# Kernel optimization log

Measured on AMD Instinct MI355X. Metric: run time of the kernel, lower is better.

## Reference

```python
import jax, jax.numpy as jnp
import numpy as np

CASCADES = 3
D, H, W = 64, 256, 256
HID = 8  # BasicBlock hidden channels


def fdiff(x, axis):
    """Forward difference D x along `axis` (last entry 0) == sparse dx/dy/dz matmul."""
    axis = axis % x.ndim
    pad = [(0, 0)] * x.ndim
    pad[axis] = (0, 1)
    return jnp.pad(jnp.diff(x, axis=axis), pad)


def fdiff_t(y, axis):
    """Exact transpose D^T y of fdiff: (D^T y)_0=-y_0, (D^T y)_j=y_{j-1}-y_j, (D^T y)_{n-1}=y_{n-2}."""
    axis = axis % y.ndim
    n = y.shape[axis]
    yl = jax.lax.slice_in_dim(y, 0, n - 1, axis=axis)  # y[0..n-2]
    pf = [(0, 0)] * y.ndim; pf[axis] = (1, 0)
    pb = [(0, 0)] * y.ndim; pb[axis] = (0, 1)
    return jnp.pad(yl, pf) - jnp.pad(yl, pb)


def conv3d(x, w, b):
    out = jax.lax.conv_general_dilated(
        x, w, window_strides=(1, 1, 1), padding='SAME',
        dimension_numbers=('NCDHW', 'OIDHW', 'NCDHW'))
    return out + b[None, :, None, None, None]


def basic_block(x, w1, b1, w2, b2):
    h = jax.nn.relu(conv3d(x, w1, b1))
    return conv3d(h, w2, b2), jnp.mean(jnp.abs(h))


def ite(t, sino):
    """BeijingGeometry stand-in: one SIRT-style step A^T(sino - A t)/D, A = sum over depth."""
    proj = jnp.sum(t, axis=2)               # [B,1,H,W]
    res = sino - proj
    return jnp.broadcast_to(res[:, :, None], t.shape) / t.shape[2]


def setup_inputs() -> dict:
    key = jax.random.key(0)
    ks = jax.random.split(key, 8)
    image = jax.random.normal(ks[0], (1, 1, D, H, W), dtype=jnp.float32)
    sino = jax.random.normal(ks[1], (1, 1, H, W), dtype=jnp.float32)
    # 4 BasicBlocks stacked on leading axis
    W1 = jax.random.normal(ks[2], (4, HID, 1, 3, 3, 3), dtype=jnp.float32) * 0.1
    B1 = jnp.zeros((4, HID), dtype=jnp.float32)
    W2 = jax.random.normal(ks[3], (4, 1, HID, 3, 3, 3), dtype=jnp.float32) * 0.1
    B2 = jnp.zeros((4, 1), dtype=jnp.float32)
    ntx = jnp.full((CASCADES,), -0.01, dtype=jnp.float32)
    nty = jnp.full((CASCADES,), -0.01, dtype=jnp.float32)
    ntz = jnp.full((CASCADES,), -0.01, dtype=jnp.float32)
    nt = jnp.full((CASCADES,), -0.1, dtype=jnp.float32)
    return {"image": image, "sino": sino, "W1": W1, "B1": B1, "W2": W2, "B2": B2,
            "ntx": ntx, "nty": nty, "ntz": ntz, "nt": nt}


def reference(image, sino, W1, B1, W2, B2, ntx, nty, ntz, nt):
    t = image
    p = q = s = jnp.float32(0.0)
    outs = [image]
    for c in range(CASCADES):
        z = t + ite(t, sino)
        pnew, _ = basic_block(fdiff(z, -1), W1[0], B1[0], W2[0], B2[0])  # d/dx (W axis)
        qnew, _ = basic_block(fdiff(z, -2), W1[1], B1[1], W2[1], B2[1])  # d/dy (H axis)
        snew, _ = basic_block(fdiff(z, -3), W1[2], B1[2], W2[2], B2[2])  # d/dz (D axis)
        znew, _ = basic_block(z, W1[3], B1[3], W2[3], B2[3])
        p = p + ntx[c] * (p - pnew)
        q = q + nty[c] * (q - qnew)
        s = s + ntz[c] * (s - snew)
        z_ = t + nt[c] * (t - znew)
        t = fdiff_t(p, -1) + fdiff_t(q, -2) + fdiff_t(s, -3) + z_
        outs.append(t)
    return jnp.stack(outs, axis=0)  # [cascades+1, B, 1, D, H, W]
```

## Files before the change

### kernel.cpp

```cpp
#include <hip/hip_runtime.h>

#define DD 64
#define HH 256
#define WW 256
#define HW (HH * WW)
#define NVOX (DD * HW)

#define TS 32
#define DR 36
#define HPH 40
#define CHB 16
#define NPF 6

typedef __fp16 half2v __attribute__((ext_vector_type(2)));

#if __has_builtin(__builtin_amdgcn_fdot2)
#define FDOT2(a, b, c) __builtin_amdgcn_fdot2((a), (b), (c), false)
#else
#define FDOT2(a, b, c) \
  fmaf((float)(a).x, (float)(b).x, fmaf((float)(a).y, (float)(b).y, (c)))
#endif

__global__ __launch_bounds__(256) void k_corr(const float* __restrict__ t,
                                              const float* __restrict__ sino,
                                              float* __restrict__ corr) {
  int idx = blockIdx.x * 256 + threadIdx.x;
  float s = 0.f;
#pragma unroll 8
  for (int d = 0; d < DD; ++d) s += t[d * HW + idx];
  corr[idx] = (sino[idx] - s) * (1.0f / DD);
}

__global__ __launch_bounds__(256, 4) void k_blocks(
    const float* __restrict__ t, const float* __restrict__ corr,
    float* __restrict__ p, float* __restrict__ q, float* __restrict__ s_,
    float* __restrict__ zb,
    const float* __restrict__ W1g, const float* __restrict__ B1g,
    const float* __restrict__ W2g, const float* __restrict__ B2g,
    const float* __restrict__ ntx, const float* __restrict__ nty,
    const float* __restrict__ ntz, const float* __restrict__ nt, int c) {
  __shared__ __align__(16) float dbuf[3][DR][DR];
  __shared__ __align__(16) __fp16 hbuf[8][34][HPH];
  __shared__ __align__(8) half2v wpkl[72];

  const int b = blockIdx.z & 3;
  const int D0 = (blockIdx.z >> 2) * CHB;
  const int Dend = (D0 + CHB < DD) ? (D0 + CHB) : DD;
  const int ty0 = blockIdx.y * TS;
  const int tx0 = blockIdx.x * TS;
  const int tid = threadIdx.x;
  const bool edgeT = (ty0 == 0) || (ty0 == HH - TS) || (tx0 == 0) || (tx0 == WW - TS);

  const float* w1 = W1g + b * 216;
  const float* w2 = W2g + b * 216;
  float b1[8];
#pragma unroll
  for (int ch = 0; ch < 8; ++ch) b1[ch] = B1g[b * 8 + ch];
  const float b2 = B2g[b];
  const float coef = (b == 0) ? ntx[c] : (b == 1) ? nty[c] : (b == 2) ? ntz[c] : nt[c];
  const float* prevBuf = (b == 0) ? p : (b == 1) ? q : (b == 2) ? s_ : t;
  float* outBuf = (b == 0) ? p : (b == 1) ? q : (b == 2) ? s_ : zb;
  const bool zeroPrev = (c == 0) && (b < 3);
  const int strideA = (b == 0) ? 1 : (b == 1) ? WW : HW;

  auto dslot = [](int f) { return (f + 6) % 3; };

  if (tid < 72) {
    int ch = tid / 9, pr = tid - ch * 9;
    const float* w = w2 + ch * 27 + pr * 3;
    half2v hv;
    hv.x = (__fp16)w[0];
    hv.y = (__fp16)w[1];
    wpkl[tid] = hv;
  }

  int cbt[NPF];
  float dC[NPF];
  unsigned mbits = 0;
#pragma unroll
  for (int k = 0; k < NPF; ++k) {
    int i = tid + k * 256;
    int iy = i / DR, ix = i - iy * DR;
    int gy = ty0 - 2 + iy, gx = tx0 - 2 + ix;
    bool inb = (i < DR * DR) && ((unsigned)gy < HH) && ((unsigned)gx < WW);
    int cb = gy * WW + gx;
    cbt[k] = cb;
    bool m;
    float d = 0.f;
    if (b == 0) {
      m = inb && (gx + 1 < WW);
      if (m) d = corr[cb + 1] - corr[cb];
    } else if (b == 1) {
      m = inb && (gy + 1 < HH);
      if (m) d = corr[cb + WW] - corr[cb];
    } else if (b == 2) {
      m = inb;
    } else {
      m = inb;
      if (m) d = corr[cb];
    }
    dC[k] = d;
    if (m) mbits |= (1u << k);
  }

  float pA0[NPF], pA1[NPF];

  auto issue_loads = [&](int f) {
    const bool fok = (f >= 0) && (f < DD) && (b != 2 || (f + 1 < DD));
    const int fb = f * HW;
#pragma unroll
    for (int k = 0; k < NPF; ++k) {
      pA0[k] = 0.f; pA1[k] = 0.f;
      if (fok && ((mbits >> k) & 1u)) {
        const float* base = t + fb + cbt[k];
        pA0[k] = base[0];
        if (b != 3) pA1[k] = base[strideA];
      }
    }
  };
  auto write_deriv = [&](int f) {
    float* dst = &dbuf[dslot(f)][0][0];
#pragma unroll
    for (int k = 0; k < NPF; ++k) {
      if (k < 5 || tid < (DR * DR - 5 * 256)) {
        float v = (b == 3) ? (pA0[k] + dC[k]) : ((pA1[k] - pA0[k]) + dC[k]);
        dst[tid + k * 256] = v;
      }
    }
  };

  auto conv1_patch = [&](const float* d0, const float* d1, const float* d2,
                         int jy, int jx, int ch0, int ch1) {
    float win[3][4][4];
#pragma unroll
    for (int r = 0; r < 4; ++r) {
      int off = (jy + r) * DR + jx;
      const float2* r0 = (const float2*)(d0 + off);
      const float2* r1 = (const float2*)(d1 + off);
      const float2* r2 = (const float2*)(d2 + off);
      float2 a, bb;
      a = r0[0]; bb = r0[1];
      win[0][r][0] = a.x; win[0][r][1] = a.y; win[0][r][2] = bb.x; win[0][r][3] = bb.y;
      a = r1[0]; bb = r1[1];
      win[1][r][0] = a.x; win[1][r][1] = a.y; win[1][r][2] = bb.x; win[1][r][3] = bb.y;
      a = r2[0]; bb = r2[1];
      win[2][r][0] = a.x; win[2][r][1] = a.y; win[2][r][2] = bb.x; win[2][r][3] = bb.y;
    }
    bool in00 = true, in01 = true, in10 = true, in11 = true;
    if (edgeT) {
      int gy0 = ty0 - 1 + jy, gx0 = tx0 - 1 + jx;
      in00 = ((unsigned)gy0 < HH) && ((unsigned)gx0 < WW);
      in01 = ((unsigned)gy0 < HH) && ((unsigned)(gx0 + 1) < WW);
      in10 = ((unsigned)(gy0 + 1) < HH) && ((unsigned)gx0 < WW);
      in11 = ((unsigned)(gy0 + 1) < HH) && ((unsigned)(gx0 + 1) < WW);
    }
#pragma unroll 2
    for (int ch = ch0; ch < ch1; ++ch) {
      float bia = b1[ch];
      float a00 = bia, a01 = bia, a10 = bia, a11 = bia;
      const float* wch = w1 + ch * 27;
#pragma unroll
      for (int kz = 0; kz < 3; ++kz)
#pragma unroll
        for (int ky = 0; ky < 3; ++ky)
#pragma unroll
          for (int kx = 0; kx < 3; ++kx) {
            float wv = wch[kz * 9 + ky * 3 + kx];
            a00 = fmaf(wv, win[kz][ky][kx], a00);
            a01 = fmaf(wv, win[kz][ky][kx + 1], a01);
            a10 = fmaf(wv, win[kz][ky + 1][kx], a10);
            a11 = fmaf(wv, win[kz][ky + 1][kx + 1], a11);
          }
      float r00 = fmaxf(a00, 0.f), r01 = fmaxf(a01, 0.f);
      float r10 = fmaxf(a10, 0.f), r11 = fmaxf(a11, 0.f);
      if (edgeT) {
        r00 = in00 ? r00 : 0.f;
        r01 = in01 ? r01 : 0.f;
        r10 = in10 ? r10 : 0.f;
        r11 = in11 ? r11 : 0.f;
      }
      half2v h0, h1;
      h0.x = (__fp16)r00; h0.y = (__fp16)r01;
      h1.x = (__fp16)r10; h1.y = (__fp16)r11;
      *(half2v*)&hbuf[ch][jy][jx] = h0;
      *(half2v*)&hbuf[ch][jy + 1][jx] = h1;
    }
  };

  auto comp_hidden = [&](int e) {
    const float* d0 = &dbuf[dslot(e - 1)][0][0];
    const float* d1 = &dbuf[dslot(e)][0][0];
    const float* d2 = &dbuf[dslot(e + 1)][0][0];
    {
      int prr = tid / 17, pcc = tid - prr * 17;
      conv1_patch(d0, d1, d2, prr * 2, pcc * 2, 0, 8);
    }
    if (tid < 132) {
      int m = tid >> 2, chp = (tid & 3) << 1;
      int pi = 256 + m;
      int prr = pi / 17, pcc = pi - prr * 17;
      conv1_patch(d0, d1, d2, prr * 2, pcc * 2, chp, chp + 2);
    }
  };

  const int txi = tid & 15, tyi = tid >> 4;
  const int px0 = txi * 2, py0 = tyi * 2;

  float aM[2][2], aC[2][2], aP[2][2];
#pragma unroll
  for (int i = 0; i < 2; ++i)
#pragma unroll
    for (int j = 0; j < 2; ++j) { aM[i][j] = b2; aC[i][j] = b2; aP[i][j] = b2; }

  issue_loads(D0 - 2); write_deriv(D0 - 2);
  issue_loads(D0 - 1); write_deriv(D0 - 1);
  issue_loads(D0);     write_deriv(D0);
  __syncthreads();

  for (int e = D0 - 1; e <= Dend; ++e) {
    const bool live = (e >= 0 && e < DD);
    issue_loads(e + 2);
    float2 pr0, pr1;
    pr0.x = pr0.y = pr1.x = pr1.y = 0.f;
    const int d = e - 1;
    const bool doStore = (e >= D0 + 1);
    if (doStore && !zeroPrev) {
      size_t v0 = (size_t)d * HW + (size_t)(ty0 + py0) * WW + tx0 + px0;
      pr0 = *(const float2*)&prevBuf[v0];
      pr1 = *(const float2*)&prevBuf[v0 + WW];
    }
    if (live) comp_hidden(e);
    __syncthreads();
    if (live) {
#pragma unroll 1
      for (int ch = 0; ch < 8; ++ch) {
        const float* wch = w2 + ch * 27;
        const half2v* wrow = &wpkl[ch * 9];
        half2v H0[4], HP[4];
        float c0[4], c1[4];
#pragma unroll
        for (int r = 0; r < 4; ++r) {
          const __fp16* hp = &hbuf[ch][py0 + r][px0];
          half2v h0 = *(const half2v*)hp;
          half2v h1 = *(const half2v*)(hp + 2);
          unsigned u0, u1;
          __builtin_memcpy(&u0, &h0, 4);
          __builtin_memcpy(&u1, &h1, 4);
          unsigned pm = (u1 << 16) | (u0 >> 16);
          half2v hpv;
          __builtin_memcpy(&hpv, &pm, 4);
          H0[r] = h0; HP[r] = hpv;
          c0[r] = (float)h1.x;
          c1[r] = (float)h1.y;
        }
#pragma unroll
        for (int ky = 0; ky < 3; ++ky)
#pragma unroll
          for (int i = 0; i < 2; ++i) {
            const int r = i + ky;
            const half2v hA = H0[r], hB = HP[r];
            const float s0 = c0[r], s1 = c1[r];
            {
              half2v wv = wrow[ky];
              float ws = wch[ky * 3 + 2];
              aP[i][0] = FDOT2(hA, wv, aP[i][0]);
              aP[i][0] = fmaf(ws, s0, aP[i][0]);
              aP[i][1] = FDOT2(hB, wv, aP[i][1]);
              aP[i][1] = fmaf(ws, s1, aP[i][1]);
            }
            {
              half2v wv = wrow[3 + ky];
              float ws = wch[9 + ky * 3 + 2];
              aC[i][0] = FDOT2(hA, wv, aC[i][0]);
              aC[i][0] = fmaf(ws, s0, aC[i][0]);
              aC[i][1] = FDOT2(hB, wv, aC[i][1]);
              aC[i][1] = fmaf(ws, s1, aC[i][1]);
            }
            {
              half2v wv = wrow[6 + ky];
              float ws = wch[18 + ky * 3 + 2];
              aM[i][0] = FDOT2(hA, wv, aM[i][0]);
              aM[i][0] = fmaf(ws, s0, aM[i][0]);
              aM[i][1] = FDOT2(hB, wv, aM[i][1]);
              aM[i][1] = fmaf(ws, s1, aM[i][1]);
            }
          }
      }
    }
    write_deriv(e + 2);
    if (doStore) {
      size_t v0 = (size_t)d * HW + (size_t)(ty0 + py0) * WW + tx0 + px0;
      float2 o0, o1;
      o0.x = pr0.x + coef * (pr0.x - aM[0][0]);
      o0.y = pr0.y + coef * (pr0.y - aM[0][1]);
      o1.x = pr1.x + coef * (pr1.x - aM[1][0]);
      o1.y = pr1.y + coef * (pr1.y - aM[1][1]);
      *(float2*)&outBuf[v0] = o0;
      *(float2*)&outBuf[v0 + WW] = o1;
    }
#pragma unroll
    for (int i = 0; i < 2; ++i)
#pragma unroll
      for (int j = 0; j < 2; ++j) {
        aM[i][j] = aC[i][j]; aC[i][j] = aP[i][j]; aP[i][j] = b2;
      }
    __syncthreads();
  }
}

__global__ __launch_bounds__(256) void k_combine(
    const float* __restrict__ p, const float* __restrict__ q,
    const float* __restrict__ s_, const float* __restrict__ zb,
    float* __restrict__ tn) {
  int idx = blockIdx.x * 256 + threadIdx.x;
  int x = idx & (WW - 1);
  int y = (idx >> 8) & (HH - 1);
  int d = idx >> 16;
  float v = zb[idx];
  v += (x > 0 ? p[idx - 1] : 0.f) - (x < WW - 1 ? p[idx] : 0.f);
  v += (y > 0 ? q[idx - WW] : 0.f) - (y < HH - 1 ? q[idx] : 0.f);
  v += (d > 0 ? s_[idx - HW] : 0.f) - (d < DD - 1 ? s_[idx] : 0.f);
  tn[idx] = v;
}

extern "C" void kernel_launch(void* const* d_in, const int* in_sizes, int n_in,
                              void* d_out, int out_size, void* d_ws, size_t ws_size,
                              hipStream_t stream) {
  const float* image = (const float*)d_in[0];
  const float* sino  = (const float*)d_in[1];
  const float* W1    = (const float*)d_in[2];
  const float* B1    = (const float*)d_in[3];
  const float* W2    = (const float*)d_in[4];
  const float* B2    = (const float*)d_in[5];
  const float* ntx   = (const float*)d_in[6];
  const float* nty   = (const float*)d_in[7];
  const float* ntz   = (const float*)d_in[8];
  const float* nt    = (const float*)d_in[9];
  float* out = (float*)d_out;

  float* corr = (float*)d_ws;
  float* p  = corr + HW;
  float* q  = p + NVOX;
  float* s_ = q + NVOX;
  float* zb = s_ + NVOX;

  hipMemcpyAsync(out, image, (size_t)NVOX * sizeof(float),
                 hipMemcpyDeviceToDevice, stream);

  for (int c = 0; c < 3; ++c) {
    const float* t = out + (size_t)c * NVOX;
    float* tn = out + (size_t)(c + 1) * NVOX;
    k_corr<<<HW / 256, 256, 0, stream>>>(t, sino, corr);
    k_blocks<<<dim3(WW / TS, HH / TS, 16), 256, 0, stream>>>(
        t, corr, p, q, s_, zb, W1, B1, W2, B2, ntx, nty, ntz, nt, c);
    k_combine<<<NVOX / 256, 256, 0, stream>>>(p, q, s_, zb, tn);
  }
}
```

Baseline: 972.0 us.

## Use 320-thread blocks so each thread computes one full conv1 patch

Raises the fused conv block size from 256 to 320 threads so that 289 threads each compute one 2x2 hidden patch for all 8 channels. This removes the uneven second pass in which 132 threads split the leftover patches across channel pairs. Only the first 256 threads do the second convolution and the stores, and the derivative staging loads are respread over 5 per-thread slots. It also switches the fp16 packing to the cvt_pkrtz intrinsic, which rounds toward zero instead of to nearest. The trade-off is 64 threads idle during conv2 and more register pressure from the new occupancy target in launch_bounds.

```diff
diff --git a/kernel.cpp b/kernel.cpp
--- a/kernel.cpp
+++ b/kernel.cpp
@@ -10,7 +10,8 @@
 #define DR 36
 #define HPH 40
 #define CHB 16
-#define NPF 6
+#define NT 320
+#define NPF 5
 
 typedef __fp16 half2v __attribute__((ext_vector_type(2)));
 
@@ -31,7 +32,7 @@
   corr[idx] = (sino[idx] - s) * (1.0f / DD);
 }
 
-__global__ __launch_bounds__(256, 4) void k_blocks(
+__global__ __launch_bounds__(NT, 5) void k_blocks(
     const float* __restrict__ t, const float* __restrict__ corr,
     float* __restrict__ p, float* __restrict__ q, float* __restrict__ s_,
     float* __restrict__ zb,
@@ -49,6 +50,7 @@
   const int ty0 = blockIdx.y * TS;
   const int tx0 = blockIdx.x * TS;
   const int tid = threadIdx.x;
+  const bool owner = (tid < 256);
   const bool edgeT = (ty0 == 0) || (ty0 == HH - TS) || (tx0 == 0) || (tx0 == WW - TS);
 
   const float* w1 = W1g + b * 216;
@@ -79,7 +81,7 @@
   unsigned mbits = 0;
 #pragma unroll
   for (int k = 0; k < NPF; ++k) {
-    int i = tid + k * 256;
+    int i = tid + k * NT;
     int iy = i / DR, ix = i - iy * DR;
     int gy = ty0 - 2 + iy, gx = tx0 - 2 + ix;
     bool inb = (i < DR * DR) && ((unsigned)gy < HH) && ((unsigned)gx < WW);
@@ -122,15 +124,15 @@
     float* dst = &dbuf[dslot(f)][0][0];
 #pragma unroll
     for (int k = 0; k < NPF; ++k) {
-      if (k < 5 || tid < (DR * DR - 5 * 256)) {
+      if (k < NPF - 1 || tid < (DR * DR - (NPF - 1) * NT)) {
         float v = (b == 3) ? (pA0[k] + dC[k]) : ((pA1[k] - pA0[k]) + dC[k]);
-        dst[tid + k * 256] = v;
+        dst[tid + k * NT] = v;
       }
     }
   };
 
   auto conv1_patch = [&](const float* d0, const float* d1, const float* d2,
-                         int jy, int jx, int ch0, int ch1) {
+                         int jy, int jx) {
     float win[3][4][4];
 #pragma unroll
     for (int r = 0; r < 4; ++r) {
@@ -155,7 +157,7 @@
       in11 = ((unsigned)(gy0 + 1) < HH) && ((unsigned)(gx0 + 1) < WW);
     }
 #pragma unroll 2
-    for (int ch = ch0; ch < ch1; ++ch) {
+    for (int ch = 0; ch < 8; ++ch) {
       float bia = b1[ch];
       float a00 = bia, a01 = bia, a10 = bia, a11 = bia;
       const float* wch = w1 + ch * 27;
@@ -179,31 +181,22 @@
         r10 = in10 ? r10 : 0.f;
         r11 = in11 ? r11 : 0.f;
       }
-      half2v h0, h1;
-      h0.x = (__fp16)r00; h0.y = (__fp16)r01;
-      h1.x = (__fp16)r10; h1.y = (__fp16)r11;
-      *(half2v*)&hbuf[ch][jy][jx] = h0;
-      *(half2v*)&hbuf[ch][jy + 1][jx] = h1;
+      *(half2v*)&hbuf[ch][jy][jx]     = __builtin_amdgcn_cvt_pkrtz(r00, r01);
+      *(half2v*)&hbuf[ch][jy + 1][jx] = __builtin_amdgcn_cvt_pkrtz(r10, r11);
     }
   };
 
   auto comp_hidden = [&](int e) {
-    const float* d0 = &dbuf[dslot(e - 1)][0][0];
-    const float* d1 = &dbuf[dslot(e)][0][0];
-    const float* d2 = &dbuf[dslot(e + 1)][0][0];
-    {
+    if (tid < 289) {
+      const float* d0 = &dbuf[dslot(e - 1)][0][0];
+      const float* d1 = &dbuf[dslot(e)][0][0];
+      const float* d2 = &dbuf[dslot(e + 1)][0][0];
       int prr = tid / 17, pcc = tid - prr * 17;
-      conv1_patch(d0, d1, d2, prr * 2, pcc * 2, 0, 8);
-    }
-    if (tid < 132) {
-      int m = tid >> 2, chp = (tid & 3) << 1;
-      int pi = 256 + m;
-      int prr = pi / 17, pcc = pi - prr * 17;
-      conv1_patch(d0, d1, d2, prr * 2, pcc * 2, chp, chp + 2);
+      conv1_patch(d0, d1, d2, prr * 2, pcc * 2);
     }
   };
 
-  const int txi = tid & 15, tyi = tid >> 4;
+  const int txi = tid & 15, tyi = (tid >> 4) & 15;
   const int px0 = txi * 2, py0 = tyi * 2;
 
   float aM[2][2], aC[2][2], aP[2][2];
@@ -223,7 +216,7 @@
     float2 pr0, pr1;
     pr0.x = pr0.y = pr1.x = pr1.y = 0.f;
     const int d = e - 1;
-    const bool doStore = (e >= D0 + 1);
+    const bool doStore = (e >= D0 + 1) && owner;
     if (doStore && !zeroPrev) {
       size_t v0 = (size_t)d * HW + (size_t)(ty0 + py0) * WW + tx0 + px0;
       pr0 = *(const float2*)&prevBuf[v0];
@@ -231,12 +224,12 @@
     }
     if (live) comp_hidden(e);
     __syncthreads();
-    if (live) {
+    if (live && owner) {
 #pragma unroll 1
       for (int ch = 0; ch < 8; ++ch) {
         const float* wch = w2 + ch * 27;
         const half2v* wrow = &wpkl[ch * 9];
-        half2v H0[4], HP[4];
+        half2v H0[4], HPv[4];
         float c0[4], c1[4];
 #pragma unroll
         for (int r = 0; r < 4; ++r) {
@@ -249,7 +242,7 @@
           unsigned pm = (u1 << 16) | (u0 >> 16);
           half2v hpv;
           __builtin_memcpy(&hpv, &pm, 4);
-          H0[r] = h0; HP[r] = hpv;
+          H0[r] = h0; HPv[r] = hpv;
           c0[r] = (float)h1.x;
           c1[r] = (float)h1.y;
         }
@@ -258,7 +251,7 @@
 #pragma unroll
           for (int i = 0; i < 2; ++i) {
             const int r = i + ky;
-            const half2v hA = H0[r], hB = HP[r];
+            const half2v hA = H0[r], hB = HPv[r];
             const float s0 = c0[r], s1 = c1[r];
             {
               half2v wv = wrow[ky];
@@ -351,7 +344,7 @@
     const float* t = out + (size_t)c * NVOX;
     float* tn = out + (size_t)(c + 1) * NVOX;
     k_corr<<<HW / 256, 256, 0, stream>>>(t, sino, corr);
-    k_blocks<<<dim3(WW / TS, HH / TS, 16), 256, 0, stream>>>(
+    k_blocks<<<dim3(WW / TS, HH / TS, 16), NT, 0, stream>>>(
         t, corr, p, q, s_, zb, W1, B1, W2, B2, ntx, nty, ntz, nt, c);
     k_combine<<<NVOX / 256, 256, 0, stream>>>(p, q, s_, zb, tn);
   }
```

New measurement: 1.183 ms. 21.7% more time.
